# Performance work log

Measured on AMD Instinct MI355X. Metric: run time of the kernel, lower is better.

The kernel has to match this reference:

```python
import jax, jax.numpy as jnp
import numpy as np

B, T = 64, 512
L, D = 2048, 512


def setup_inputs() -> dict:
    key = jax.random.key(0)
    k1, k2, k3 = jax.random.split(key, 3)
    label_sequences = jax.random.randint(k1, (B, T), 0, L)
    source_embeddings = jax.random.normal(k2, (L, D), dtype=jnp.float32)
    target_embeddings = jax.random.normal(k3, (L, D), dtype=jnp.float32)
    return {
        "label_sequences": label_sequences,
        "source_embeddings": source_embeddings,
        "target_embeddings": target_embeddings,
    }


def reference(label_sequences, source_embeddings, target_embeddings):
    # source_index = labels[:, :-1], target_index = labels[:, 1:]
    src_idx = label_sequences[:, :-1]          # [B, T-1]
    tgt_idx = label_sequences[:, 1:]           # [B, T-1]
    # Gather source embeddings per transition pair: [B, T-1, D]
    src = source_embeddings[src_idx]
    # Logits over all target labels: [B, T-1, L]
    logits = jnp.einsum("btd,ld->btl", src, target_embeddings)
    # Row-wise log_softmax over target labels (dim=1 in torch == last axis here)
    logp = jax.nn.log_softmax(logits, axis=-1)
    # Pick the actual next label's log-probability: [B, T-1]
    scores = jnp.take_along_axis(logp, tgt_idx[..., None], axis=-1)[..., 0]
    return scores
```

## Files before the change

kernel.cpp:

```cpp
#include <hip/hip_runtime.h>
#include <hip/hip_bf16.h>

#define L_CLS 2048
#define D_DIM 512
#define T_SZ  512
#define NT    511
#define NOUT  (64 * NT)
#define NCHUNK 16
#define LDS_STRIDE 136
#define LOG2E 1.4426950408889634f
#define LN2   0.6931471805599453f
#define SHIFT 128.0f

typedef __attribute__((ext_vector_type(8))) short bf16x8;
typedef __attribute__((ext_vector_type(4))) float f32x4;

static __device__ __forceinline__ short f2bf(float x) {
    return (short)__bfloat16_as_ushort(__float2bfloat16(x));
}

__launch_bounds__(256)
__global__ void gemm_lse(const float* __restrict__ srcE,
                         const float* __restrict__ tgtE,
                         float* __restrict__ psum,
                         float* __restrict__ M, int useM) {
    __shared__ __hip_bfloat16 Blds[128 * LDS_STRIDE];

    const int tid  = threadIdx.x;
    const int wave = tid >> 6;
    const int lane = tid & 63;
    const int lr   = lane & 15;
    const int hi   = lane >> 4;
    const int by   = blockIdx.x;
    const int bx   = blockIdx.y;
    const int C    = by * 128;
    const int R0   = bx * 64 + wave * 16;
    const int R1   = (bx + 16) * 64 + wave * 16;

    f32x4 acc[2][8];
#pragma unroll
    for (int rb = 0; rb < 2; ++rb)
#pragma unroll
        for (int ct = 0; ct < 8; ++ct) acc[rb][ct] = (f32x4){0.f, 0.f, 0.f, 0.f};

#pragma unroll 1
    for (int s = 0; s < 4; ++s) {
#pragma unroll
        for (int i = 0; i < 8; ++i) {
            int p   = tid + 256 * i;
            int row = p >> 4;
            int grp = p & 15;
            const f32x4* g = reinterpret_cast<const f32x4*>(
                tgtE + (C + row) * D_DIM + s * 128 + grp * 8);
            f32x4 x0 = g[0], x1 = g[1];
            bf16x8 v;
#pragma unroll
            for (int e = 0; e < 4; ++e) { v[e] = f2bf(x0[e]); v[e + 4] = f2bf(x1[e]); }
            *reinterpret_cast<bf16x8*>(&Blds[row * LDS_STRIDE + grp * 8]) = v;
        }
        __syncthreads();

        bf16x8 a[2][4];
#pragma unroll
        for (int rb = 0; rb < 2; ++rb) {
            const int R = rb ? R1 : R0;
            const float* arow = srcE + (R + lr) * D_DIM + s * 128 + hi * 8;
#pragma unroll
            for (int ks = 0; ks < 4; ++ks) {
                const f32x4* g = reinterpret_cast<const f32x4*>(arow + ks * 32);
                f32x4 x0 = g[0], x1 = g[1];
                bf16x8 v;
#pragma unroll
                for (int e = 0; e < 4; ++e) { v[e] = f2bf(x0[e]); v[e + 4] = f2bf(x1[e]); }
                a[rb][ks] = v;
            }
        }

#pragma unroll
        for (int ks = 0; ks < 4; ++ks) {
            const int off = ks * 32 + hi * 8;
#pragma unroll
            for (int ct = 0; ct < 8; ++ct) {
                bf16x8 b = *reinterpret_cast<const bf16x8*>(
                    &Blds[(ct * 16 + lr) * LDS_STRIDE + off]);
                acc[0][ct] = __builtin_amdgcn_mfma_f32_16x16x32_bf16(a[0][ks], b, acc[0][ct], 0, 0, 0);
                acc[1][ct] = __builtin_amdgcn_mfma_f32_16x16x32_bf16(a[1][ks], b, acc[1][ct], 0, 0, 0);
            }
        }
        __syncthreads();
    }

#pragma unroll
    for (int rb = 0; rb < 2; ++rb) {
        const int R = rb ? R1 : R0;
        if (useM) {
#pragma unroll
            for (int i = 0; i < 4; ++i) {
                size_t rg = (size_t)(R + hi * 4 + i) * L_CLS + C + lr;
#pragma unroll
                for (int ct = 0; ct < 8; ++ct)
                    M[rg + ct * 16] = acc[rb][ct][i];
            }
        }
        float p[4];
#pragma unroll
        for (int i = 0; i < 4; ++i) {
            p[i] = 0.f;
#pragma unroll
            for (int ct = 0; ct < 8; ++ct)
                p[i] += exp2f(acc[rb][ct][i] * LOG2E - SHIFT);
        }
#pragma unroll
        for (int off = 1; off < 16; off <<= 1)
#pragma unroll
            for (int i = 0; i < 4; ++i) p[i] += __shfl_xor(p[i], off);
        if (lr == 0) {
#pragma unroll
            for (int i = 0; i < 4; ++i)
                psum[(R + hi * 4 + i) * NCHUNK + by] = p[i];
        }
    }
}

__launch_bounds__(256)
__global__ void scores_gather(const int* __restrict__ labels,
                              const float* __restrict__ psum,
                              const float* __restrict__ M,
                              float* __restrict__ out) {
    int o = blockIdx.x * 256 + threadIdx.x;
    if (o >= NOUT) return;
    int b = o / NT;
    int t = o - b * NT;
    int src = labels[b * T_SZ + t];
    int tgt = labels[b * T_SZ + t + 1];

    const f32x4* pv = reinterpret_cast<const f32x4*>(psum + src * NCHUNK);
    f32x4 s0 = pv[0], s1 = pv[1], s2 = pv[2], s3 = pv[3];
    float S = (s0[0]+s0[1]+s0[2]+s0[3]) + (s1[0]+s1[1]+s1[2]+s1[3])
            + (s2[0]+s2[1]+s2[2]+s2[3]) + (s3[0]+s3[1]+s3[2]+s3[3]);
    float lse = (log2f(S) + SHIFT) * LN2;
    out[o] = M[(size_t)src * L_CLS + tgt] - lse;
}

__launch_bounds__(256)
__global__ void scores_dot(const int* __restrict__ labels,
                           const float* __restrict__ srcE,
                           const float* __restrict__ tgtE,
                           const float* __restrict__ psum,
                           float* __restrict__ out) {
    const int wid  = blockIdx.x * 4 + (threadIdx.x >> 6);
    const int lane = threadIdx.x & 63;
    const int b = wid / NT;
    const int t = wid - b * NT;
    const int src = labels[b * T_SZ + t];
    const int tgt = labels[b * T_SZ + t + 1];

    const f32x4* sp = reinterpret_cast<const f32x4*>(srcE + src * D_DIM + lane * 8);
    const f32x4* tp = reinterpret_cast<const f32x4*>(tgtE + tgt * D_DIM + lane * 8);
    f32x4 s0 = sp[0], s1 = sp[1];
    f32x4 t0 = tp[0], t1 = tp[1];
    float acc = 0.f;
#pragma unroll
    for (int j = 0; j < 4; ++j) acc += s0[j] * t0[j] + s1[j] * t1[j];
    float ps = (lane < NCHUNK) ? psum[src * NCHUNK + lane] : 0.f;
#pragma unroll
    for (int off = 32; off; off >>= 1) {
        acc += __shfl_xor(acc, off);
        ps  += __shfl_xor(ps, off);
    }
    if (lane == 0) out[wid] = acc - (log2f(ps) + SHIFT) * LN2;
}

extern "C" void kernel_launch(void* const* d_in, const int* in_sizes, int n_in,
                              void* d_out, int out_size, void* d_ws, size_t ws_size,
                              hipStream_t stream) {
    const int*   labels = (const int*)d_in[0];
    const float* srcE   = (const float*)d_in[1];
    const float* tgtE   = (const float*)d_in[2];
    float*       out    = (float*)d_out;

    float* psum = (float*)d_ws;
    float* M    = psum + L_CLS * NCHUNK;

    size_t need = ((size_t)L_CLS * NCHUNK + (size_t)L_CLS * L_CLS) * sizeof(float);
    int useM = (ws_size >= need) ? 1 : 0;

    gemm_lse<<<dim3(NCHUNK, 16), 256, 0, stream>>>(srcE, tgtE, psum, M, useM);
    if (useM)
        scores_gather<<<(NOUT + 255) / 256, 256, 0, stream>>>(labels, psum, M, out);
    else
        scores_dot<<<NOUT / 4, 256, 0, stream>>>(labels, srcE, tgtE, psum, out);
}
```

Baseline: 31.62 us.

## Pre-convert embeddings to bf16 and software-pipeline GEMM loads with larger blocks

Adds a separate kernel that converts both embedding tables to bf16 once. The GEMM then loads bf16 operands directly, register-prefetching the next K-slab of B and A while the current one is computed, and uses 512-thread blocks with one row-block per wave instead of two. This removes the repeated fp32 loads and conversions inside the GEMM and hides global latency behind the MFMA work. In exchange it adds an extra kernel launch, an extra bf16 round trip through workspace, and a larger workspace requirement. The old fp32 path is kept as a fallback.

```diff
diff --git a/kernel.cpp b/kernel.cpp
--- a/kernel.cpp
+++ b/kernel.cpp
@@ -19,11 +19,29 @@
     return (short)__bfloat16_as_ushort(__float2bfloat16(x));
 }
 
-__launch_bounds__(256)
-__global__ void gemm_lse(const float* __restrict__ srcE,
-                         const float* __restrict__ tgtE,
-                         float* __restrict__ psum,
-                         float* __restrict__ M, int useM) {
+__global__ void conv_bf16(const float* __restrict__ srcE, const float* __restrict__ tgtE,
+                          __hip_bfloat16* __restrict__ Sb, __hip_bfloat16* __restrict__ Tb) {
+    int i = blockIdx.x * blockDim.x + threadIdx.x;
+    if (i >= (L_CLS * D_DIM) / 8) return;
+    const f32x4* s4 = reinterpret_cast<const f32x4*>(srcE) + i * 2;
+    const f32x4* t4 = reinterpret_cast<const f32x4*>(tgtE) + i * 2;
+    f32x4 s0 = s4[0], s1 = s4[1];
+    f32x4 t0 = t4[0], t1 = t4[1];
+    bf16x8 so, to;
+#pragma unroll
+    for (int j = 0; j < 4; ++j) {
+        so[j] = f2bf(s0[j]); so[j + 4] = f2bf(s1[j]);
+        to[j] = f2bf(t0[j]); to[j + 4] = f2bf(t1[j]);
+    }
+    reinterpret_cast<bf16x8*>(Sb)[i] = so;
+    reinterpret_cast<bf16x8*>(Tb)[i] = to;
+}
+
+__launch_bounds__(512)
+__global__ void gemm_lse_bf16(const __hip_bfloat16* __restrict__ Sb,
+                              const __hip_bfloat16* __restrict__ Tb,
+                              float* __restrict__ psum,
+                              float* __restrict__ M) {
     __shared__ __hip_bfloat16 Blds[128 * LDS_STRIDE];
 
     const int tid  = threadIdx.x;
@@ -31,49 +49,48 @@
     const int lane = tid & 63;
     const int lr   = lane & 15;
     const int hi   = lane >> 4;
-    const int by   = blockIdx.x;
-    const int bx   = blockIdx.y;
-    const int C    = by * 128;
-    const int R0   = bx * 64 + wave * 16;
-    const int R1   = (bx + 16) * 64 + wave * 16;
-
-    f32x4 acc[2][8];
-#pragma unroll
-    for (int rb = 0; rb < 2; ++rb)
-#pragma unroll
-        for (int ct = 0; ct < 8; ++ct) acc[rb][ct] = (f32x4){0.f, 0.f, 0.f, 0.f};
+    const int C    = blockIdx.x * 128;
+    const int R    = blockIdx.y * 128 + wave * 16;
+
+    f32x4 acc[8];
+#pragma unroll
+    for (int ct = 0; ct < 8; ++ct) acc[ct] = (f32x4){0.f, 0.f, 0.f, 0.f};
+
+    bf16x8 stg[4], an[4];
+#pragma unroll
+    for (int i = 0; i < 4; ++i) {
+        int p = tid + 512 * i;
+        stg[i] = *reinterpret_cast<const bf16x8*>(
+            &Tb[(C + (p >> 4)) * D_DIM + (p & 15) * 8]);
+    }
+#pragma unroll
+    for (int ks = 0; ks < 4; ++ks)
+        an[ks] = *reinterpret_cast<const bf16x8*>(
+            &Sb[(R + lr) * D_DIM + ks * 32 + hi * 8]);
 
 #pragma unroll 1
     for (int s = 0; s < 4; ++s) {
 #pragma unroll
-        for (int i = 0; i < 8; ++i) {
-            int p   = tid + 256 * i;
-            int row = p >> 4;
-            int grp = p & 15;
-            const f32x4* g = reinterpret_cast<const f32x4*>(
-                tgtE + (C + row) * D_DIM + s * 128 + grp * 8);
-            f32x4 x0 = g[0], x1 = g[1];
-            bf16x8 v;
-#pragma unroll
-            for (int e = 0; e < 4; ++e) { v[e] = f2bf(x0[e]); v[e + 4] = f2bf(x1[e]); }
-            *reinterpret_cast<bf16x8*>(&Blds[row * LDS_STRIDE + grp * 8]) = v;
-        }
+        for (int i = 0; i < 4; ++i) {
+            int p = tid + 512 * i;
+            *reinterpret_cast<bf16x8*>(&Blds[(p >> 4) * LDS_STRIDE + (p & 15) * 8]) = stg[i];
+        }
+        bf16x8 a[4];
+#pragma unroll
+        for (int ks = 0; ks < 4; ++ks) a[ks] = an[ks];
         __syncthreads();
 
-        bf16x8 a[2][4];
-#pragma unroll
-        for (int rb = 0; rb < 2; ++rb) {
-            const int R = rb ? R1 : R0;
-            const float* arow = srcE + (R + lr) * D_DIM + s * 128 + hi * 8;
-#pragma unroll
-            for (int ks = 0; ks < 4; ++ks) {
-                const f32x4* g = reinterpret_cast<const f32x4*>(arow + ks * 32);
-                f32x4 x0 = g[0], x1 = g[1];
-                bf16x8 v;
-#pragma unroll
-                for (int e = 0; e < 4; ++e) { v[e] = f2bf(x0[e]); v[e + 4] = f2bf(x1[e]); }
-                a[rb][ks] = v;
-            }
+        if (s < 3) {
+#pragma unroll
+            for (int i = 0; i < 4; ++i) {
+                int p = tid + 512 * i;
+                stg[i] = *reinterpret_cast<const bf16x8*>(
+                    &Tb[(C + (p >> 4)) * D_DIM + (s + 1) * 128 + (p & 15) * 8]);
+            }
+#pragma unroll
+            for (int ks = 0; ks < 4; ++ks)
+                an[ks] = *reinterpret_cast<const bf16x8*>(
+                    &Sb[(R + lr) * D_DIM + (s + 1) * 128 + ks * 32 + hi * 8]);
         }
 
 #pragma unroll
@@ -83,42 +100,35 @@
             for (int ct = 0; ct < 8; ++ct) {
                 bf16x8 b = *reinterpret_cast<const bf16x8*>(
                     &Blds[(ct * 16 + lr) * LDS_STRIDE + off]);
-                acc[0][ct] = __builtin_amdgcn_mfma_f32_16x16x32_bf16(a[0][ks], b, acc[0][ct], 0, 0, 0);
-                acc[1][ct] = __builtin_amdgcn_mfma_f32_16x16x32_bf16(a[1][ks], b, acc[1][ct], 0, 0, 0);
+                acc[ct] = __builtin_amdgcn_mfma_f32_16x16x32_bf16(a[ks], b, acc[ct], 0, 0, 0);
             }
         }
         __syncthreads();
     }
 
 #pragma unroll
-    for (int rb = 0; rb < 2; ++rb) {
-        const int R = rb ? R1 : R0;
-        if (useM) {
-#pragma unroll
-            for (int i = 0; i < 4; ++i) {
-                size_t rg = (size_t)(R + hi * 4 + i) * L_CLS + C + lr;
-#pragma unroll
-                for (int ct = 0; ct < 8; ++ct)
-                    M[rg + ct * 16] = acc[rb][ct][i];
-            }
-        }
-        float p[4];
-#pragma unroll
-        for (int i = 0; i < 4; ++i) {
-            p[i] = 0.f;
-#pragma unroll
-            for (int ct = 0; ct < 8; ++ct)
-                p[i] += exp2f(acc[rb][ct][i] * LOG2E - SHIFT);
-        }
-#pragma unroll
-        for (int off = 1; off < 16; off <<= 1)
-#pragma unroll
-            for (int i = 0; i < 4; ++i) p[i] += __shfl_xor(p[i], off);
-        if (lr == 0) {
-#pragma unroll
-            for (int i = 0; i < 4; ++i)
-                psum[(R + hi * 4 + i) * NCHUNK + by] = p[i];
-        }
+    for (int i = 0; i < 4; ++i) {
+        size_t rg = (size_t)(R + hi * 4 + i) * L_CLS + C + lr;
+#pragma unroll
+        for (int ct = 0; ct < 8; ++ct)
+            M[rg + ct * 16] = acc[ct][i];
+    }
+    float p[4];
+#pragma unroll
+    for (int i = 0; i < 4; ++i) {
+        p[i] = 0.f;
+#pragma unroll
+        for (int ct = 0; ct < 8; ++ct)
+            p[i] += exp2f(acc[ct][i] * LOG2E - SHIFT);
+    }
+#pragma unroll
+    for (int off = 1; off < 16; off <<= 1)
+#pragma unroll
+        for (int i = 0; i < 4; ++i) p[i] += __shfl_xor(p[i], off);
+    if (lr == 0) {
+#pragma unroll
+        for (int i = 0; i < 4; ++i)
+            psum[(R + hi * 4 + i) * NCHUNK + blockIdx.x] = p[i];
     }
 }
 
@@ -140,6 +150,97 @@
             + (s2[0]+s2[1]+s2[2]+s2[3]) + (s3[0]+s3[1]+s3[2]+s3[3]);
     float lse = (log2f(S) + SHIFT) * LN2;
     out[o] = M[(size_t)src * L_CLS + tgt] - lse;
+}
+
+__launch_bounds__(256)
+__global__ void gemm_lse_f32(const float* __restrict__ srcE,
+                             const float* __restrict__ tgtE,
+                             float* __restrict__ psum,
+                             float* __restrict__ M, int useM) {
+    __shared__ __hip_bfloat16 Blds[128 * LDS_STRIDE];
+    const int tid  = threadIdx.x;
+    const int wave = tid >> 6;
+    const int lane = tid & 63;
+    const int lr   = lane & 15;
+    const int hi   = lane >> 4;
+    const int C    = blockIdx.x * 128;
+    const int R0   = blockIdx.y * 64 + wave * 16;
+    const int R1   = (blockIdx.y + 16) * 64 + wave * 16;
+
+    f32x4 acc[2][8];
+#pragma unroll
+    for (int rb = 0; rb < 2; ++rb)
+#pragma unroll
+        for (int ct = 0; ct < 8; ++ct) acc[rb][ct] = (f32x4){0.f, 0.f, 0.f, 0.f};
+
+#pragma unroll 1
+    for (int s = 0; s < 4; ++s) {
+#pragma unroll
+        for (int i = 0; i < 8; ++i) {
+            int p = tid + 256 * i, row = p >> 4, grp = p & 15;
+            const f32x4* g = reinterpret_cast<const f32x4*>(
+                tgtE + (C + row) * D_DIM + s * 128 + grp * 8);
+            f32x4 x0 = g[0], x1 = g[1];
+            bf16x8 v;
+#pragma unroll
+            for (int e = 0; e < 4; ++e) { v[e] = f2bf(x0[e]); v[e + 4] = f2bf(x1[e]); }
+            *reinterpret_cast<bf16x8*>(&Blds[row * LDS_STRIDE + grp * 8]) = v;
+        }
+        __syncthreads();
+        bf16x8 a[2][4];
+#pragma unroll
+        for (int rb = 0; rb < 2; ++rb) {
+            const float* arow = srcE + ((rb ? R1 : R0) + lr) * D_DIM + s * 128 + hi * 8;
+#pragma unroll
+            for (int ks = 0; ks < 4; ++ks) {
+                const f32x4* g = reinterpret_cast<const f32x4*>(arow + ks * 32);
+                f32x4 x0 = g[0], x1 = g[1];
+                bf16x8 v;
+#pragma unroll
+                for (int e = 0; e < 4; ++e) { v[e] = f2bf(x0[e]); v[e + 4] = f2bf(x1[e]); }
+                a[rb][ks] = v;
+            }
+        }
+#pragma unroll
+        for (int ks = 0; ks < 4; ++ks) {
+            const int off = ks * 32 + hi * 8;
+#pragma unroll
+            for (int ct = 0; ct < 8; ++ct) {
+                bf16x8 b = *reinterpret_cast<const bf16x8*>(&Blds[(ct * 16 + lr) * LDS_STRIDE + off]);
+                acc[0][ct] = __builtin_amdgcn_mfma_f32_16x16x32_bf16(a[0][ks], b, acc[0][ct], 0, 0, 0);
+                acc[1][ct] = __builtin_amdgcn_mfma_f32_16x16x32_bf16(a[1][ks], b, acc[1][ct], 0, 0, 0);
+            }
+        }
+        __syncthreads();
+    }
+#pragma unroll
+    for (int rb = 0; rb < 2; ++rb) {
+        const int R = rb ? R1 : R0;
+        if (useM) {
+#pragma unroll
+            for (int i = 0; i < 4; ++i) {
+                size_t rg = (size_t)(R + hi * 4 + i) * L_CLS + C + lr;
+#pragma unroll
+                for (int ct = 0; ct < 8; ++ct) M[rg + ct * 16] = acc[rb][ct][i];
+            }
+        }
+        float p[4];
+#pragma unroll
+        for (int i = 0; i < 4; ++i) {
+            p[i] = 0.f;
+#pragma unroll
+            for (int ct = 0; ct < 8; ++ct) p[i] += exp2f(acc[rb][ct][i] * LOG2E - SHIFT);
+        }
+#pragma unroll
+        for (int off = 1; off < 16; off <<= 1)
+#pragma unroll
+            for (int i = 0; i < 4; ++i) p[i] += __shfl_xor(p[i], off);
+        if (lr == 0) {
+#pragma unroll
+            for (int i = 0; i < 4; ++i)
+                psum[(R + hi * 4 + i) * NCHUNK + blockIdx.x] = p[i];
+        }
+    }
 }
 
 __launch_bounds__(256)
@@ -154,7 +255,6 @@
     const int t = wid - b * NT;
     const int src = labels[b * T_SZ + t];
     const int tgt = labels[b * T_SZ + t + 1];
-
     const f32x4* sp = reinterpret_cast<const f32x4*>(srcE + src * D_DIM + lane * 8);
     const f32x4* tp = reinterpret_cast<const f32x4*>(tgtE + tgt * D_DIM + lane * 8);
     f32x4 s0 = sp[0], s1 = sp[1];
@@ -179,15 +279,28 @@
     const float* tgtE   = (const float*)d_in[2];
     float*       out    = (float*)d_out;
 
-    float* psum = (float*)d_ws;
-    float* M    = psum + L_CLS * NCHUNK;
-
-    size_t need = ((size_t)L_CLS * NCHUNK + (size_t)L_CLS * L_CLS) * sizeof(float);
-    int useM = (ws_size >= need) ? 1 : 0;
-
-    gemm_lse<<<dim3(NCHUNK, 16), 256, 0, stream>>>(srcE, tgtE, psum, M, useM);
-    if (useM)
+    const size_t tbl = (size_t)L_CLS * D_DIM;
+    const size_t needBF = 2 * tbl * sizeof(__hip_bfloat16)
+                        + (size_t)L_CLS * NCHUNK * sizeof(float)
+                        + (size_t)L_CLS * L_CLS * sizeof(float);
+
+    if (ws_size >= needBF) {
+        __hip_bfloat16* Sb = (__hip_bfloat16*)d_ws;
+        __hip_bfloat16* Tb = Sb + tbl;
+        float* psum = (float*)((char*)d_ws + 2 * tbl * sizeof(__hip_bfloat16));
+        float* M    = psum + (size_t)L_CLS * NCHUNK;
+        conv_bf16<<<(int)(tbl / 8 + 255) / 256, 256, 0, stream>>>(srcE, tgtE, Sb, Tb);
+        gemm_lse_bf16<<<dim3(NCHUNK, 16), 512, 0, stream>>>(Sb, Tb, psum, M);
         scores_gather<<<(NOUT + 255) / 256, 256, 0, stream>>>(labels, psum, M, out);
-    else
-        scores_dot<<<NOUT / 4, 256, 0, stream>>>(labels, srcE, tgtE, psum, out);
-}
+    } else {
+        float* psum = (float*)d_ws;
+        float* M    = psum + (size_t)L_CLS * NCHUNK;
+        size_t need = ((size_t)L_CLS * NCHUNK + (size_t)L_CLS * L_CLS) * sizeof(float);
+        int useM = (ws_size >= need) ? 1 : 0;
+        gemm_lse_f32<<<dim3(NCHUNK, 16), 256, 0, stream>>>(srcE, tgtE, psum, M, useM);
+        if (useM)
+            scores_gather<<<(NOUT + 255) / 256, 256, 0, stream>>>(labels, psum, M, out);
+        else
+            scores_dot<<<NOUT / 4, 256, 0, stream>>>(labels, srcE, tgtE, psum, out);
+    }
+}
```

Measured after the change: 27.60 us. 12.7% less time.
